# Optimization experiments

Measured on AMD Instinct MI355X. Metric: run time of the kernel, lower is better.

## Reference

```python
import jax, jax.numpy as jnp
import numpy as np
from jax import lax

B, T, H, F, K, NB, MAXLEN = 32, 1024, 384, 384, 3, 256, 2048


def _ln(x, g, b, eps=1e-5):
    m = jnp.mean(x, axis=-1, keepdims=True)
    v = jnp.var(x, axis=-1, keepdims=True)
    return (x - m) * lax.rsqrt(v + eps) * g + b


def _conv(x, w, b):
    # x: (B, T, Cin), w: (K, Cin, Cout); SAME padding == torch padding=(K-1)//2 for K=3, stride 1
    y = lax.conv_general_dilated(x, w, (1,), 'SAME', dimension_numbers=('NWC', 'WIO', 'NWC'))
    return y + b


def _predictor(x, mask, w1, b1, g1, be1, w2, b2, g2, be2, wo, bo):
    h = _ln(jax.nn.relu(_conv(x, w1, b1)), g1, be1)
    h = _ln(jax.nn.relu(_conv(h, w2, b2)), g2, be2)
    out = jnp.einsum('btf,f->bt', h, wo) + bo  # Linear(F -> 1).squeeze(-1)
    return jnp.where(mask, 0.0, out)


def _length_regulate(x, dur, max_len):
    # vectorized equivalent of torch per-sample expand+cat+pad
    csum = jnp.cumsum(dur, axis=1)                      # (B, T)
    total = csum[:, -1]                                 # (B,) = mel_len
    frames = jnp.arange(max_len)                        # (M,)
    # frame f belongs to phoneme i with csum[i-1] <= f < csum[i]
    idx = jax.vmap(lambda c: jnp.searchsorted(c, frames, side='right'))(csum)  # (B, M)
    idx = jnp.clip(idx, 0, x.shape[1] - 1)
    out = jnp.take_along_axis(x, idx[:, :, None], axis=1)                      # (B, M, H)
    valid = (frames[None, :] < total[:, None]).astype(x.dtype)                 # zero-pad tail
    return out * valid[:, :, None], total


def setup_inputs() -> dict:
    key = jax.random.key(0)
    ks = iter(jax.random.split(key, 64))
    nk = lambda: next(ks)
    d = {}
    d['x'] = jax.random.normal(nk(), (B, T, H), jnp.float32)
    d['src_mask'] = jnp.zeros((B, T), jnp.bool_)
    d['duration'] = jax.random.randint(nk(), (B, T), 0, 4)
    d['max_len'] = MAXLEN
    for p in ('dp', 'pp', 'ep'):
        d[p + '_w1'] = jax.random.normal(nk(), (K, H, F), jnp.float32) * 0.02
        d[p + '_b1'] = jnp.zeros((F,), jnp.float32)
        d[p + '_g1'] = jnp.ones((F,), jnp.float32)
        d[p + '_be1'] = jnp.zeros((F,), jnp.float32)
        d[p + '_w2'] = jax.random.normal(nk(), (K, F, F), jnp.float32) * 0.02
        d[p + '_b2'] = jnp.zeros((F,), jnp.float32)
        d[p + '_g2'] = jnp.ones((F,), jnp.float32)
        d[p + '_be2'] = jnp.zeros((F,), jnp.float32)
        d[p + '_wo'] = jax.random.normal(nk(), (F,), jnp.float32) * 0.02
        d[p + '_bo'] = jnp.zeros((1,), jnp.float32)
    d['pitch_bins'] = jnp.linspace(0.0, 1.0, NB - 1, dtype=jnp.float32)
    d['energy_bins'] = jnp.linspace(0.0, 1.0, NB - 1, dtype=jnp.float32)
    d['pitch_emb'] = jax.random.normal(nk(), (NB, H), jnp.float32) * 0.02
    d['energy_emb'] = jax.random.normal(nk(), (NB, H), jnp.float32) * 0.02
    d['pitch_target'] = jax.random.uniform(nk(), (B, T), jnp.float32)
    d['energy_target'] = jax.random.uniform(nk(), (B, T), jnp.float32)
    return d


def reference(x, src_mask, duration, max_len,
              dp_w1, dp_b1, dp_g1, dp_be1, dp_w2, dp_b2, dp_g2, dp_be2, dp_wo, dp_bo,
              pp_w1, pp_b1, pp_g1, pp_be1, pp_w2, pp_b2, pp_g2, pp_be2, pp_wo, pp_bo,
              ep_w1, ep_b1, ep_g1, ep_be1, ep_w2, ep_b2, ep_g2, ep_be2, ep_wo, ep_bo,
              pitch_bins, energy_bins, pitch_emb, energy_emb, pitch_target, energy_target):
    log_dur = _predictor(x, src_mask, dp_w1, dp_b1, dp_g1, dp_be1, dp_w2, dp_b2, dp_g2, dp_be2, dp_wo, dp_bo)
    # phoneme-level pitch (target path: bucketize target, torch.bucketize right=False == searchsorted left)
    pitch_pred = _predictor(x, src_mask, pp_w1, pp_b1, pp_g1, pp_be1, pp_w2, pp_b2, pp_g2, pp_be2, pp_wo, pp_bo)
    x = x + pitch_emb[jnp.searchsorted(pitch_bins, pitch_target, side='left')]
    # phoneme-level energy (predictor sees x AFTER pitch embedding add, as in torch)
    energy_pred = _predictor(x, src_mask, ep_w1, ep_b1, ep_g1, ep_be1, ep_w2, ep_b2, ep_g2, ep_be2, ep_wo, ep_bo)
    x = x + energy_emb[jnp.searchsorted(energy_bins, energy_target, side='left')]
    x_out, mel_len = _length_regulate(x, duration, max_len)
    return (x_out, pitch_pred, energy_pred, log_dur, mel_len)
```

## Files before the change

### kernel.cpp

```cpp
#include <hip/hip_runtime.h>

#define B_ 32
#define T_ 1024
#define C_ 384
#define MAXLEN_ 2048
#define NBINS_ 255
#define WPK1 442368
#define BTC  (32 * 1024 * 384)
#define ARS 392

typedef __attribute__((ext_vector_type(8))) short short8v;
typedef __attribute__((ext_vector_type(4))) float floatx4;

__device__ __forceinline__ unsigned short f2bf(float f) {
    unsigned u = __float_as_uint(f);
    u += 0x7fffu + ((u >> 16) & 1u);
    return (unsigned short)(u >> 16);
}

struct CvP {
    const float* xf;
    const unsigned short* xb;
    const unsigned short* wpk;
    const float* bias[3];
    const float* gamma[3];
    const float* beta[3];
    const float* wo[3];
    const float* bo[3];
    unsigned short* hout;
    float* pred[3];
    const float* pbins;
    const float* pemb;
    const float* ptgt;
    int final_flag;
};

__global__ __launch_bounds__(256, 2) void conv_mfma3(CvP P)
{
    __shared__ unsigned short As[66 * ARS];
    float* rsum = (float*)As;
    float* rsq  = rsum + 256;

    const int tid  = threadIdx.x;
    const int wave = tid >> 6;
    const int lane = tid & 63;
    const int lq   = lane >> 4;
    const int ln   = lane & 15;
    const int p    = blockIdx.x >> 9;
    const int bi   = blockIdx.x & 511;
    const int b    = bi >> 4;
    const int t0   = (bi & 15) << 6;
    const int nb   = wave * 96;

    const unsigned short* bbase =
        P.wpk + (size_t)p * WPK1 + wave * 3072 + (size_t)lane * 8;
    short8v bA[6], bB[6];
#pragma unroll
    for (int nt = 0; nt < 6; ++nt) {
        bA[nt] = *(const short8v*)(bbase + (nt << 9));
        bB[nt] = *(const short8v*)(bbase + 12288 + (nt << 9));
    }

    if (!P.final_flag) {
        const bool fuse_emb = (p == 2);
        for (int i = tid; i < 66 * 48; i += 256) {
            const int row = i / 48;
            const int c   = i - row * 48;
            const int t   = t0 - 1 + row;
            short8v v = (short8v){0,0,0,0,0,0,0,0};
            if ((unsigned)t < (unsigned)T_) {
                const float* sp = P.xf + ((size_t)(b << 10) + t) * C_ + c * 8;
                float f[8];
                *(float4*)&f[0] = *(const float4*)sp;
                *(float4*)&f[4] = *(const float4*)(sp + 4);
                if (fuse_emb) {
                    const float tg = P.ptgt[(b << 10) + t];
                    int lo = 0, hi = NBINS_;
                    while (lo < hi) {
                        const int mid = (lo + hi) >> 1;
                        if (P.pbins[mid] < tg) lo = mid + 1; else hi = mid;
                    }
                    const float* er = P.pemb + (size_t)lo * C_ + c * 8;
#pragma unroll
                    for (int j = 0; j < 8; ++j) f[j] += er[j];
                }
#pragma unroll
                for (int j = 0; j < 8; ++j) v[j] = (short)f2bf(f[j]);
            }
            *(short8v*)&As[row * ARS + c * 8] = v;
        }
    } else {
        const unsigned short* xb = P.xb + (size_t)p * BTC;
        for (int i = tid; i < 66 * 48; i += 256) {
            const int row = i / 48;
            const int c   = i - row * 48;
            const int t   = t0 - 1 + row;
            short8v v = (short8v){0,0,0,0,0,0,0,0};
            if ((unsigned)t < (unsigned)T_)
                v = *(const short8v*)(xb + ((size_t)(b << 10) + t) * C_ + c * 8);
            *(short8v*)&As[row * ARS + c * 8] = v;
        }
    }
    __syncthreads();

    floatx4 acc[24];
#pragma unroll
    for (int i = 0; i < 24; ++i) acc[i] = (floatx4){0.f, 0.f, 0.f, 0.f};

    const unsigned short* abase = &As[ln * ARS + lq * 8];
    const unsigned short* bpA = bbase + 2 * 12288;
    const unsigned short* bpB = bbase + 3 * 12288;

#pragma unroll
    for (int kc = 0; kc < 3; ++kc) {
#pragma unroll
        for (int h2 = 0; h2 < 6; ++h2) {
            const int hb = h2 * 64;
            const int r  = kc * 12 + h2 * 2;
            {
                short8v afrag[4];
#pragma unroll
                for (int mt = 0; mt < 4; ++mt)
                    afrag[mt] = *(const short8v*)(abase + (mt * 16 + kc) * ARS + hb);
#pragma unroll
                for (int mt = 0; mt < 4; ++mt)
#pragma unroll
                    for (int nt = 0; nt < 6; ++nt)
                        acc[mt * 6 + nt] = __builtin_amdgcn_mfma_f32_16x16x32_bf16(
                            afrag[mt], bA[nt], acc[mt * 6 + nt], 0, 0, 0);
                if (r + 2 < 36) {
#pragma unroll
                    for (int nt = 0; nt < 6; ++nt)
                        bA[nt] = *(const short8v*)(bpA + (nt << 9));
                    bpA += 24576;
                }
            }
            {
                short8v afrag[4];
#pragma unroll
                for (int mt = 0; mt < 4; ++mt)
                    afrag[mt] = *(const short8v*)(abase + (mt * 16 + kc) * ARS + hb + 32);
#pragma unroll
                for (int mt = 0; mt < 4; ++mt)
#pragma unroll
                    for (int nt = 0; nt < 6; ++nt)
                        acc[mt * 6 + nt] = __builtin_amdgcn_mfma_f32_16x16x32_bf16(
                            afrag[mt], bB[nt], acc[mt * 6 + nt], 0, 0, 0);
                if (r + 3 < 36) {
#pragma unroll
                    for (int nt = 0; nt < 6; ++nt)
                        bB[nt] = *(const short8v*)(bpB + (nt << 9));
                    bpB += 24576;
                }
            }
        }
    }
    __syncthreads();

    float bcol[6], gcol[6], becol[6], wcol[6];
#pragma unroll
    for (int nt = 0; nt < 6; ++nt) {
        const int col = nb + nt * 16 + ln;
        bcol[nt]  = P.bias[p][col];
        gcol[nt]  = P.gamma[p][col];
        becol[nt] = P.beta[p][col];
        wcol[nt]  = P.final_flag ? P.wo[p][col] : 0.f;
    }

#pragma unroll
    for (int mt = 0; mt < 4; ++mt) {
#pragma unroll
        for (int rg = 0; rg < 4; ++rg) {
            float s = 0.f, q = 0.f;
#pragma unroll
            for (int nt = 0; nt < 6; ++nt) {
                float v = acc[mt * 6 + nt][rg] + bcol[nt];
                v = v > 0.f ? v : 0.f;
                acc[mt * 6 + nt][rg] = v;
                s += v; q += v * v;
            }
#pragma unroll
            for (int off = 1; off < 16; off <<= 1) {
                s += __shfl_xor(s, off, 64);
                q += __shfl_xor(q, off, 64);
            }
            if (ln == mt * 4 + rg) {
                rsum[wave * 64 + mt * 16 + lq * 4 + rg] = s;
                rsq [wave * 64 + mt * 16 + lq * 4 + rg] = q;
            }
        }
    }
    __syncthreads();

    float mean_[16], rstd_[16];
#pragma unroll
    for (int mt = 0; mt < 4; ++mt) {
#pragma unroll
        for (int rg = 0; rg < 4; ++rg) {
            const int row = mt * 16 + lq * 4 + rg;
            const float s = rsum[row] + rsum[64 + row] + rsum[128 + row] + rsum[192 + row];
            const float q = rsq[row] + rsq[64 + row] + rsq[128 + row] + rsq[192 + row];
            const float m = s * (1.f / 384.f);
            const float var = q * (1.f / 384.f) - m * m;
            mean_[mt * 4 + rg] = m;
            rstd_[mt * 4 + rg] = rsqrtf(var + 1e-5f);
        }
    }

    if (!P.final_flag) {
        unsigned short* hout = P.hout + (size_t)p * BTC;
#pragma unroll
        for (int mt = 0; mt < 4; ++mt)
#pragma unroll
            for (int rg = 0; rg < 4; ++rg) {
                const float m = mean_[mt * 4 + rg], rs = rstd_[mt * 4 + rg];
                const int grow = (bi << 6) + mt * 16 + lq * 4 + rg;
#pragma unroll
                for (int nt = 0; nt < 6; ++nt) {
                    const float v = (acc[mt * 6 + nt][rg] - m) * rs * gcol[nt] + becol[nt];
                    hout[(size_t)grow * C_ + nb + nt * 16 + ln] = f2bf(v);
                }
            }
    } else {
        __syncthreads();
#pragma unroll
        for (int mt = 0; mt < 4; ++mt) {
#pragma unroll
            for (int rg = 0; rg < 4; ++rg) {
                const float m = mean_[mt * 4 + rg], rs = rstd_[mt * 4 + rg];
                float pr = 0.f;
#pragma unroll
                for (int nt = 0; nt < 6; ++nt)
                    pr += ((acc[mt * 6 + nt][rg] - m) * rs * gcol[nt] + becol[nt]) * wcol[nt];
#pragma unroll
                for (int off = 1; off < 16; off <<= 1)
                    pr += __shfl_xor(pr, off, 64);
                if (ln == mt * 4 + rg)
                    rsum[wave * 64 + mt * 16 + lq * 4 + rg] = pr;
            }
        }
        __syncthreads();
        if (tid < 64)
            P.pred[p][(bi << 6) + tid] =
                rsum[tid] + rsum[64 + tid] + rsum[128 + tid] + rsum[192 + tid] + P.bo[p][0];
    }
}

__global__ __launch_bounds__(256) void pack_w_kernel(
    const float* __restrict__ s0, const float* __restrict__ s1,
    const float* __restrict__ s2, const float* __restrict__ s3,
    const float* __restrict__ s4, const float* __restrict__ s5,
    unsigned short* __restrict__ dst)
{
    const int wsel = blockIdx.y;
    const float* src = wsel == 0 ? s0 : wsel == 1 ? s1 : wsel == 2 ? s2
                     : wsel == 3 ? s3 : wsel == 4 ? s4 : s5;
    const int o = blockIdx.x * 256 + threadIdx.x;
    const int r    = o / 12288;
    const int rem  = o - r * 12288;
    const int wv   = rem / 3072;
    const int rem2 = rem - wv * 3072;
    const int nt   = rem2 >> 9;
    const int li   = rem2 & 511;
    const int lane = li >> 3;
    const int j    = li & 7;
    const int n = wv * 96 + nt * 16 + (lane & 15);
    const int k = ((lane >> 4) << 3) + j;
    dst[(size_t)wsel * WPK1 + o] = f2bf(src[(size_t)(r * 32 + k) * C_ + n]);
}

__global__ __launch_bounds__(256) void cumsum_kernel(
    const int* __restrict__ dur, int* __restrict__ csum,
    float* __restrict__ mel_len)
{
    __shared__ int part[256];
    const int b = blockIdx.x;
    const int tid = threadIdx.x;
    int l[4];
    int s = 0;
#pragma unroll
    for (int i = 0; i < 4; ++i) { l[i] = dur[b * T_ + tid * 4 + i]; s += l[i]; }
    part[tid] = s;
    __syncthreads();
    for (int off = 1; off < 256; off <<= 1) {
        int u = 0;
        if (tid >= off) u = part[tid - off];
        __syncthreads();
        part[tid] += u;
        __syncthreads();
    }
    const int incl = part[tid];
    int run = incl - s;
#pragma unroll
    for (int i = 0; i < 4; ++i) {
        run += l[i];
        csum[b * T_ + tid * 4 + i] = run;
    }
    if (tid == 255) mel_len[b] = (float)incl;
}

__global__ __launch_bounds__(256) void length_reg_kernel(
    const float* __restrict__ x, const int* __restrict__ csum,
    const float* __restrict__ pbins, const float* __restrict__ pemb,
    const float* __restrict__ ptgt,
    const float* __restrict__ ebins, const float* __restrict__ eemb,
    const float* __restrict__ etgt,
    float* __restrict__ out)
{
    const int g    = blockIdx.x * 256 + threadIdx.x;
    const int c4   = g % 96;
    const int rest = g / 96;
    const int frame = rest & (MAXLEN_ - 1);
    const int b     = rest >> 11;
    const int* cr = csum + (b << 10);
    const int total = cr[T_ - 1];
    float4 v = make_float4(0.f, 0.f, 0.f, 0.f);
    if (frame < total) {
        int lo = 0, hi = T_;
        while (lo < hi) {
            const int mid = (lo + hi) >> 1;
            if (cr[mid] <= frame) lo = mid + 1; else hi = mid;
        }
        const int t = lo > T_ - 1 ? T_ - 1 : lo;
        const int row = (b << 10) + t;
        v = *(const float4*)(x + (size_t)row * C_ + c4 * 4);
        const float ptg = ptgt[row];
        int plo = 0, phi = NBINS_;
        while (plo < phi) {
            const int mid = (plo + phi) >> 1;
            if (pbins[mid] < ptg) plo = mid + 1; else phi = mid;
        }
        const float etg = etgt[row];
        int elo = 0, ehi = NBINS_;
        while (elo < ehi) {
            const int mid = (elo + ehi) >> 1;
            if (ebins[mid] < etg) elo = mid + 1; else ehi = mid;
        }
        const float4 pe = *(const float4*)(pemb + (size_t)plo * C_ + c4 * 4);
        const float4 ee = *(const float4*)(eemb + (size_t)elo * C_ + c4 * 4);
        v.x += pe.x + ee.x; v.y += pe.y + ee.y;
        v.z += pe.z + ee.z; v.w += pe.w + ee.w;
    }
    *(float4*)(out + (size_t)g * 4) = v;
}

extern "C" void kernel_launch(void* const* d_in, const int* in_sizes, int n_in,
                              void* d_out, int out_size, void* d_ws, size_t ws_size,
                              hipStream_t stream)
{
    const float* x        = (const float*)d_in[0];
    const int*   duration = (const int*)d_in[2];
    const float* P[3][10];
    for (int p = 0; p < 3; ++p)
        for (int q = 0; q < 10; ++q)
            P[p][q] = (const float*)d_in[4 + p * 10 + q];
    const float* pitch_bins    = (const float*)d_in[34];
    const float* energy_bins   = (const float*)d_in[35];
    const float* pitch_emb     = (const float*)d_in[36];
    const float* energy_emb    = (const float*)d_in[37];
    const float* pitch_target  = (const float*)d_in[38];
    const float* energy_target = (const float*)d_in[39];

    float* out_x      = (float*)d_out;
    float* out_pitch  = out_x + (size_t)B_ * MAXLEN_ * C_;
    float* out_energy = out_pitch + B_ * T_;
    float* out_logdur = out_energy + B_ * T_;
    float* out_mellen = out_logdur + B_ * T_;

    unsigned short* h1b = (unsigned short*)out_x;

    unsigned short* wpk = (unsigned short*)d_ws;
    int* csum = (int*)(wpk + (size_t)6 * WPK1);

    const dim3 blk(256);

    pack_w_kernel<<<dim3(1728, 6), blk, 0, stream>>>(
        P[0][0], P[0][4], P[1][0], P[1][4], P[2][0], P[2][4], wpk);

    CvP P1;
    P1.xf = x; P1.xb = nullptr; P1.wpk = wpk;
    for (int p = 0; p < 3; ++p) {
        P1.bias[p]  = P[p][1];
        P1.gamma[p] = P[p][2];
        P1.beta[p]  = P[p][3];
        P1.wo[p]    = nullptr;
        P1.bo[p]    = nullptr;
        P1.pred[p]  = nullptr;
    }
    P1.hout = h1b;
    P1.pbins = pitch_bins; P1.pemb = pitch_emb; P1.ptgt = pitch_target;
    P1.final_flag = 0;

    CvP P2;
    P2.xf = nullptr; P2.xb = h1b; P2.wpk = wpk + (size_t)3 * WPK1;
    for (int p = 0; p < 3; ++p) {
        P2.bias[p]  = P[p][5];
        P2.gamma[p] = P[p][6];
        P2.beta[p]  = P[p][7];
        P2.wo[p]    = P[p][8];
        P2.bo[p]    = P[p][9];
    }
    P2.pred[0] = out_logdur; P2.pred[1] = out_pitch; P2.pred[2] = out_energy;
    P2.hout = nullptr;
    P2.pbins = nullptr; P2.pemb = nullptr; P2.ptgt = nullptr;
    P2.final_flag = 1;

    conv_mfma3<<<1536, blk, 0, stream>>>(P1);
    conv_mfma3<<<1536, blk, 0, stream>>>(P2);

    cumsum_kernel<<<B_, blk, 0, stream>>>(duration, csum, out_mellen);
    length_reg_kernel<<<24576, blk, 0, stream>>>(
        x, csum, pitch_bins, pitch_emb, pitch_target,
        energy_bins, energy_emb, energy_target, out_x);
}
```

Baseline: 502.0 us.

## Single-buffer B fragments per column tile to raise occupancy to three blocks per CU

Replaces the double-buffered B-fragment registers (bA/bB) with one set that is refilled per column tile right after its MFMAs, roughly halving B register use. The launch bound rises to 3 blocks per CU to exploit the lower register pressure. The LDS row stride moves from 392 to 396 shorts to change the bank-conflict pattern. In exchange, weight loads are issued closer to their use, which gives less latency hiding within a wave and relies on the extra occupancy to cover it.

```diff
diff --git a/kernel.cpp b/kernel.cpp
--- a/kernel.cpp
+++ b/kernel.cpp
@@ -7,7 +7,7 @@
 #define NBINS_ 255
 #define WPK1 442368
 #define BTC  (32 * 1024 * 384)
-#define ARS 392
+#define ARS 396
 
 typedef __attribute__((ext_vector_type(8))) short short8v;
 typedef __attribute__((ext_vector_type(4))) float floatx4;
@@ -35,7 +35,7 @@
     int final_flag;
 };
 
-__global__ __launch_bounds__(256, 2) void conv_mfma3(CvP P)
+__global__ __launch_bounds__(256, 3) void conv_mfma3(CvP P)
 {
     __shared__ unsigned short As[66 * ARS];
     float* rsum = (float*)As;
@@ -54,12 +54,10 @@
 
     const unsigned short* bbase =
         P.wpk + (size_t)p * WPK1 + wave * 3072 + (size_t)lane * 8;
-    short8v bA[6], bB[6];
-#pragma unroll
-    for (int nt = 0; nt < 6; ++nt) {
-        bA[nt] = *(const short8v*)(bbase + (nt << 9));
-        bB[nt] = *(const short8v*)(bbase + 12288 + (nt << 9));
-    }
+    short8v bcur[6];
+#pragma unroll
+    for (int nt = 0; nt < 6; ++nt)
+        bcur[nt] = *(const short8v*)(bbase + (nt << 9));
 
     if (!P.final_flag) {
         const bool fuse_emb = (p == 2);
@@ -108,51 +106,28 @@
     for (int i = 0; i < 24; ++i) acc[i] = (floatx4){0.f, 0.f, 0.f, 0.f};
 
     const unsigned short* abase = &As[ln * ARS + lq * 8];
-    const unsigned short* bpA = bbase + 2 * 12288;
-    const unsigned short* bpB = bbase + 3 * 12288;
+    const unsigned short* bp = bbase + 12288;
 
 #pragma unroll
     for (int kc = 0; kc < 3; ++kc) {
 #pragma unroll
-        for (int h2 = 0; h2 < 6; ++h2) {
-            const int hb = h2 * 64;
-            const int r  = kc * 12 + h2 * 2;
-            {
-                short8v afrag[4];
+        for (int hh = 0; hh < 12; ++hh) {
+            const int r  = kc * 12 + hh;
+            const int hb = hh * 32;
+            short8v afrag[4];
+#pragma unroll
+            for (int mt = 0; mt < 4; ++mt)
+                afrag[mt] = *(const short8v*)(abase + (mt * 16 + kc) * ARS + hb);
+#pragma unroll
+            for (int nt = 0; nt < 6; ++nt) {
 #pragma unroll
                 for (int mt = 0; mt < 4; ++mt)
-                    afrag[mt] = *(const short8v*)(abase + (mt * 16 + kc) * ARS + hb);
-#pragma unroll
-                for (int mt = 0; mt < 4; ++mt)
-#pragma unroll
-                    for (int nt = 0; nt < 6; ++nt)
-                        acc[mt * 6 + nt] = __builtin_amdgcn_mfma_f32_16x16x32_bf16(
-                            afrag[mt], bA[nt], acc[mt * 6 + nt], 0, 0, 0);
-                if (r + 2 < 36) {
-#pragma unroll
-                    for (int nt = 0; nt < 6; ++nt)
-                        bA[nt] = *(const short8v*)(bpA + (nt << 9));
-                    bpA += 24576;
-                }
-            }
-            {
-                short8v afrag[4];
-#pragma unroll
-                for (int mt = 0; mt < 4; ++mt)
-                    afrag[mt] = *(const short8v*)(abase + (mt * 16 + kc) * ARS + hb + 32);
-#pragma unroll
-                for (int mt = 0; mt < 4; ++mt)
-#pragma unroll
-                    for (int nt = 0; nt < 6; ++nt)
-                        acc[mt * 6 + nt] = __builtin_amdgcn_mfma_f32_16x16x32_bf16(
-                            afrag[mt], bB[nt], acc[mt * 6 + nt], 0, 0, 0);
-                if (r + 3 < 36) {
-#pragma unroll
-                    for (int nt = 0; nt < 6; ++nt)
-                        bB[nt] = *(const short8v*)(bpB + (nt << 9));
-                    bpB += 24576;
-                }
-            }
+                    acc[mt * 6 + nt] = __builtin_amdgcn_mfma_f32_16x16x32_bf16(
+                        afrag[mt], bcur[nt], acc[mt * 6 + nt], 0, 0, 0);
+                if (r + 1 < 36)
+                    bcur[nt] = *(const short8v*)(bp + (nt << 9));
+            }
+            bp += 12288;
         }
     }
     __syncthreads();
```

New measurement: 586.5 us. 1.17x slower.

## Split conv tile across 8 waves and precompute length-regulator gather indices

Applied to the files above, without the earlier changes.

The conv kernel now runs 512 threads per block, with each of 8 waves owning 48 output columns instead of 96. This halves the accumulators per thread so more waves can be resident to hide latency, and the LDS row stride is padded differently. The cumsum kernel now does the frame-to-phoneme and bucketize binary searches once per frame and packs the results into an index buffer. The length-regulate kernel then only gathers, instead of repeating the searches for each of the 96 column threads. The cost is LayerNorm reductions over 8 partials and an extra index buffer in the workspace.

```diff
diff --git a/kernel.cpp b/kernel.cpp
--- a/kernel.cpp
+++ b/kernel.cpp
@@ -7,7 +7,7 @@
 #define NBINS_ 255
 #define WPK1 442368
 #define BTC  (32 * 1024 * 384)
-#define ARS 392
+#define ARS 396
 
 typedef __attribute__((ext_vector_type(8))) short short8v;
 typedef __attribute__((ext_vector_type(4))) float floatx4;
@@ -35,11 +35,11 @@
     int final_flag;
 };
 
-__global__ __launch_bounds__(256, 2) void conv_mfma3(CvP P)
+__global__ __launch_bounds__(512, 4) void conv_mfma3(CvP P)
 {
     __shared__ unsigned short As[66 * ARS];
     float* rsum = (float*)As;
-    float* rsq  = rsum + 256;
+    float* rsq  = rsum + 512;
 
     const int tid  = threadIdx.x;
     const int wave = tid >> 6;
@@ -50,20 +50,20 @@
     const int bi   = blockIdx.x & 511;
     const int b    = bi >> 4;
     const int t0   = (bi & 15) << 6;
-    const int nb   = wave * 96;
-
-    const unsigned short* bbase =
-        P.wpk + (size_t)p * WPK1 + wave * 3072 + (size_t)lane * 8;
-    short8v bA[6], bB[6];
-#pragma unroll
-    for (int nt = 0; nt < 6; ++nt) {
+    const int nb   = wave * 48;
+
+    const unsigned short* bbase = P.wpk + (size_t)p * WPK1
+        + (wave >> 1) * 3072 + (wave & 1) * 1536 + (size_t)lane * 8;
+    short8v bA[3], bB[3];
+#pragma unroll
+    for (int nt = 0; nt < 3; ++nt) {
         bA[nt] = *(const short8v*)(bbase + (nt << 9));
         bB[nt] = *(const short8v*)(bbase + 12288 + (nt << 9));
     }
 
     if (!P.final_flag) {
         const bool fuse_emb = (p == 2);
-        for (int i = tid; i < 66 * 48; i += 256) {
+        for (int i = tid; i < 66 * 48; i += 512) {
             const int row = i / 48;
             const int c   = i - row * 48;
             const int t   = t0 - 1 + row;
@@ -91,7 +91,7 @@
         }
     } else {
         const unsigned short* xb = P.xb + (size_t)p * BTC;
-        for (int i = tid; i < 66 * 48; i += 256) {
+        for (int i = tid; i < 66 * 48; i += 512) {
             const int row = i / 48;
             const int c   = i - row * 48;
             const int t   = t0 - 1 + row;
@@ -103,9 +103,9 @@
     }
     __syncthreads();
 
-    floatx4 acc[24];
-#pragma unroll
-    for (int i = 0; i < 24; ++i) acc[i] = (floatx4){0.f, 0.f, 0.f, 0.f};
+    floatx4 acc[12];
+#pragma unroll
+    for (int i = 0; i < 12; ++i) acc[i] = (floatx4){0.f, 0.f, 0.f, 0.f};
 
     const unsigned short* abase = &As[ln * ARS + lq * 8];
     const unsigned short* bpA = bbase + 2 * 12288;
@@ -125,12 +125,12 @@
 #pragma unroll
                 for (int mt = 0; mt < 4; ++mt)
 #pragma unroll
-                    for (int nt = 0; nt < 6; ++nt)
-                        acc[mt * 6 + nt] = __builtin_amdgcn_mfma_f32_16x16x32_bf16(
-                            afrag[mt], bA[nt], acc[mt * 6 + nt], 0, 0, 0);
+                    for (int nt = 0; nt < 3; ++nt)
+                        acc[mt * 3 + nt] = __builtin_amdgcn_mfma_f32_16x16x32_bf16(
+                            afrag[mt], bA[nt], acc[mt * 3 + nt], 0, 0, 0);
                 if (r + 2 < 36) {
 #pragma unroll
-                    for (int nt = 0; nt < 6; ++nt)
+                    for (int nt = 0; nt < 3; ++nt)
                         bA[nt] = *(const short8v*)(bpA + (nt << 9));
                     bpA += 24576;
                 }
@@ -143,12 +143,12 @@
 #pragma unroll
                 for (int mt = 0; mt < 4; ++mt)
 #pragma unroll
-                    for (int nt = 0; nt < 6; ++nt)
-                        acc[mt * 6 + nt] = __builtin_amdgcn_mfma_f32_16x16x32_bf16(
-                            afrag[mt], bB[nt], acc[mt * 6 + nt], 0, 0, 0);
+                    for (int nt = 0; nt < 3; ++nt)
+                        acc[mt * 3 + nt] = __builtin_amdgcn_mfma_f32_16x16x32_bf16(
+                            afrag[mt], bB[nt], acc[mt * 3 + nt], 0, 0, 0);
                 if (r + 3 < 36) {
 #pragma unroll
-                    for (int nt = 0; nt < 6; ++nt)
+                    for (int nt = 0; nt < 3; ++nt)
                         bB[nt] = *(const short8v*)(bpB + (nt << 9));
                     bpB += 24576;
                 }
@@ -157,9 +157,9 @@
     }
     __syncthreads();
 
-    float bcol[6], gcol[6], becol[6], wcol[6];
-#pragma unroll
-    for (int nt = 0; nt < 6; ++nt) {
+    float bcol[3], gcol[3], becol[3], wcol[3];
+#pragma unroll
+    for (int nt = 0; nt < 3; ++nt) {
         const int col = nb + nt * 16 + ln;
         bcol[nt]  = P.bias[p][col];
         gcol[nt]  = P.gamma[p][col];
@@ -173,10 +173,10 @@
         for (int rg = 0; rg < 4; ++rg) {
             float s = 0.f, q = 0.f;
 #pragma unroll
-            for (int nt = 0; nt < 6; ++nt) {
-                float v = acc[mt * 6 + nt][rg] + bcol[nt];
+            for (int nt = 0; nt < 3; ++nt) {
+                float v = acc[mt * 3 + nt][rg] + bcol[nt];
                 v = v > 0.f ? v : 0.f;
-                acc[mt * 6 + nt][rg] = v;
+                acc[mt * 3 + nt][rg] = v;
                 s += v; q += v * v;
             }
 #pragma unroll
@@ -198,8 +198,9 @@
 #pragma unroll
         for (int rg = 0; rg < 4; ++rg) {
             const int row = mt * 16 + lq * 4 + rg;
-            const float s = rsum[row] + rsum[64 + row] + rsum[128 + row] + rsum[192 + row];
-            const float q = rsq[row] + rsq[64 + row] + rsq[128 + row] + rsq[192 + row];
+            float s = 0.f, q = 0.f;
+#pragma unroll
+            for (int w = 0; w < 8; ++w) { s += rsum[w * 64 + row]; q += rsq[w * 64 + row]; }
             const float m = s * (1.f / 384.f);
             const float var = q * (1.f / 384.f) - m * m;
             mean_[mt * 4 + rg] = m;
@@ -216,8 +217,8 @@
                 const float m = mean_[mt * 4 + rg], rs = rstd_[mt * 4 + rg];
                 const int grow = (bi << 6) + mt * 16 + lq * 4 + rg;
 #pragma unroll
-                for (int nt = 0; nt < 6; ++nt) {
-                    const float v = (acc[mt * 6 + nt][rg] - m) * rs * gcol[nt] + becol[nt];
+                for (int nt = 0; nt < 3; ++nt) {
+                    const float v = (acc[mt * 3 + nt][rg] - m) * rs * gcol[nt] + becol[nt];
                     hout[(size_t)grow * C_ + nb + nt * 16 + ln] = f2bf(v);
                 }
             }
@@ -230,8 +231,8 @@
                 const float m = mean_[mt * 4 + rg], rs = rstd_[mt * 4 + rg];
                 float pr = 0.f;
 #pragma unroll
-                for (int nt = 0; nt < 6; ++nt)
-                    pr += ((acc[mt * 6 + nt][rg] - m) * rs * gcol[nt] + becol[nt]) * wcol[nt];
+                for (int nt = 0; nt < 3; ++nt)
+                    pr += ((acc[mt * 3 + nt][rg] - m) * rs * gcol[nt] + becol[nt]) * wcol[nt];
 #pragma unroll
                 for (int off = 1; off < 16; off <<= 1)
                     pr += __shfl_xor(pr, off, 64);
@@ -240,9 +241,12 @@
             }
         }
         __syncthreads();
-        if (tid < 64)
-            P.pred[p][(bi << 6) + tid] =
-                rsum[tid] + rsum[64 + tid] + rsum[128 + tid] + rsum[192 + tid] + P.bo[p][0];
+        if (tid < 64) {
+            float s = P.bo[p][0];
+#pragma unroll
+            for (int w = 0; w < 8; ++w) s += rsum[w * 64 + tid];
+            P.pred[p][(bi << 6) + tid] = s;
+        }
     }
 }
 
@@ -269,17 +273,22 @@
     dst[(size_t)wsel * WPK1 + o] = f2bf(src[(size_t)(r * 32 + k) * C_ + n]);
 }
 
-__global__ __launch_bounds__(256) void cumsum_kernel(
-    const int* __restrict__ dur, int* __restrict__ csum,
-    float* __restrict__ mel_len)
+__global__ __launch_bounds__(256) void cumsum_idx_kernel(
+    const int* __restrict__ dur,
+    const float* __restrict__ pbins, const float* __restrict__ ptgt,
+    const float* __restrict__ ebins, const float* __restrict__ etgt,
+    int* __restrict__ xidx, float* __restrict__ mel_len)
 {
+    __shared__ int cs[T_];
     __shared__ int part[256];
+    __shared__ float pb[NBINS_], eb[NBINS_];
     const int b = blockIdx.x;
     const int tid = threadIdx.x;
+    if (tid < NBINS_) { pb[tid] = pbins[tid]; eb[tid] = ebins[tid]; }
     int l[4];
     int s = 0;
 #pragma unroll
-    for (int i = 0; i < 4; ++i) { l[i] = dur[b * T_ + tid * 4 + i]; s += l[i]; }
+    for (int i = 0; i < 4; ++i) { l[i] = dur[(b << 10) + tid * 4 + i]; s += l[i]; }
     part[tid] = s;
     __syncthreads();
     for (int off = 1; off < 256; off <<= 1) {
@@ -294,17 +303,42 @@
 #pragma unroll
     for (int i = 0; i < 4; ++i) {
         run += l[i];
-        csum[b * T_ + tid * 4 + i] = run;
+        cs[tid * 4 + i] = run;
     }
     if (tid == 255) mel_len[b] = (float)incl;
+    __syncthreads();
+    const int total = cs[T_ - 1];
+    for (int f = tid; f < MAXLEN_; f += 256) {
+        int pk = -1;
+        if (f < total) {
+            int lo = 0, hi = T_;
+            while (lo < hi) {
+                const int mid = (lo + hi) >> 1;
+                if (cs[mid] <= f) lo = mid + 1; else hi = mid;
+            }
+            const int t = lo > T_ - 1 ? T_ - 1 : lo;
+            const int row = (b << 10) + t;
+            const float ptg = ptgt[row];
+            int plo = 0, phi = NBINS_;
+            while (plo < phi) {
+                const int mid = (plo + phi) >> 1;
+                if (pb[mid] < ptg) plo = mid + 1; else phi = mid;
+            }
+            const float etg = etgt[row];
+            int elo = 0, ehi = NBINS_;
+            while (elo < ehi) {
+                const int mid = (elo + ehi) >> 1;
+                if (eb[mid] < etg) elo = mid + 1; else ehi = mid;
+            }
+            pk = t | (plo << 10) | (elo << 19);
+        }
+        xidx[(b << 11) + f] = pk;
+    }
 }
 
 __global__ __launch_bounds__(256) void length_reg_kernel(
-    const float* __restrict__ x, const int* __restrict__ csum,
-    const float* __restrict__ pbins, const float* __restrict__ pemb,
-    const float* __restrict__ ptgt,
-    const float* __restrict__ ebins, const float* __restrict__ eemb,
-    const float* __restrict__ etgt,
+    const float* __restrict__ x, const int* __restrict__ xidx,
+    const float* __restrict__ pemb, const float* __restrict__ eemb,
     float* __restrict__ out)
 {
     const int g    = blockIdx.x * 256 + threadIdx.x;
@@ -312,30 +346,13 @@
     const int rest = g / 96;
     const int frame = rest & (MAXLEN_ - 1);
     const int b     = rest >> 11;
-    const int* cr = csum + (b << 10);
-    const int total = cr[T_ - 1];
+    const int pk = xidx[(b << 11) + frame];
     float4 v = make_float4(0.f, 0.f, 0.f, 0.f);
-    if (frame < total) {
-        int lo = 0, hi = T_;
-        while (lo < hi) {
-            const int mid = (lo + hi) >> 1;
-            if (cr[mid] <= frame) lo = mid + 1; else hi = mid;
-        }
-        const int t = lo > T_ - 1 ? T_ - 1 : lo;
-        const int row = (b << 10) + t;
-        v = *(const float4*)(x + (size_t)row * C_ + c4 * 4);
-        const float ptg = ptgt[row];
-        int plo = 0, phi = NBINS_;
-        while (plo < phi) {
-            const int mid = (plo + phi) >> 1;
-            if (pbins[mid] < ptg) plo = mid + 1; else phi = mid;
-        }
-        const float etg = etgt[row];
-        int elo = 0, ehi = NBINS_;
-        while (elo < ehi) {
-            const int mid = (elo + ehi) >> 1;
-            if (ebins[mid] < etg) elo = mid + 1; else ehi = mid;
-        }
+    if (pk >= 0) {
+        const int t   = pk & 1023;
+        const int plo = (pk >> 10) & 511;
+        const int elo = (pk >> 19) & 511;
+        v = *(const float4*)(x + ((size_t)(b << 10) + t) * C_ + c4 * 4);
         const float4 pe = *(const float4*)(pemb + (size_t)plo * C_ + c4 * 4);
         const float4 ee = *(const float4*)(eemb + (size_t)elo * C_ + c4 * 4);
         v.x += pe.x + ee.x; v.y += pe.y + ee.y;
@@ -370,7 +387,7 @@
     unsigned short* h1b = (unsigned short*)out_x;
 
     unsigned short* wpk = (unsigned short*)d_ws;
-    int* csum = (int*)(wpk + (size_t)6 * WPK1);
+    int* xidx = (int*)(wpk + (size_t)6 * WPK1);
 
     const dim3 blk(256);
 
@@ -405,11 +422,12 @@
     P2.pbins = nullptr; P2.pemb = nullptr; P2.ptgt = nullptr;
     P2.final_flag = 1;
 
-    conv_mfma3<<<1536, blk, 0, stream>>>(P1);
-    conv_mfma3<<<1536, blk, 0, stream>>>(P2);
-
-    cumsum_kernel<<<B_, blk, 0, stream>>>(duration, csum, out_mellen);
+    conv_mfma3<<<1536, dim3(512), 0, stream>>>(P1);
+    conv_mfma3<<<1536, dim3(512), 0, stream>>>(P2);
+
+    cumsum_idx_kernel<<<B_, blk, 0, stream>>>(
+        duration, pitch_bins, pitch_target, energy_bins, energy_target,
+        xidx, out_mellen);
     length_reg_kernel<<<24576, blk, 0, stream>>>(
-        x, csum, pitch_bins, pitch_emb, pitch_target,
-        energy_bins, energy_emb, energy_target, out_x);
-}
+        x, xidx, pitch_emb, energy_emb, out_x);
+}
```

Result: slower. 759.5 us (+51.3%).

## Precompute per-frame gather indices once and coalesce weight packing via LDS

Applied to the files above, without the earlier changes.

The binary searches for frame-to-phoneme mapping and pitch/energy bucketization move out of the length-regulate kernel, which ran them for each of 96 channel chunks per frame. They now run once per frame in the cumsum kernel, which writes a packed index array. The gather kernel then only decodes that index and does the loads. Separately, weight packing stages a 32-row slab in shared memory so global reads are coalesced float4 and writes are 16-byte bf16 vectors, replacing strided scalar gathers.

```diff
diff --git a/kernel.cpp b/kernel.cpp
--- a/kernel.cpp
+++ b/kernel.cpp
@@ -246,40 +246,64 @@
     }
 }
 
+#define WSS 388
 __global__ __launch_bounds__(256) void pack_w_kernel(
     const float* __restrict__ s0, const float* __restrict__ s1,
     const float* __restrict__ s2, const float* __restrict__ s3,
     const float* __restrict__ s4, const float* __restrict__ s5,
     unsigned short* __restrict__ dst)
 {
-    const int wsel = blockIdx.y;
+    __shared__ float ws[32 * WSS];
+    const int blk  = blockIdx.x;
+    const int wsel = blk / 36;
+    const int r    = blk - wsel * 36;
     const float* src = wsel == 0 ? s0 : wsel == 1 ? s1 : wsel == 2 ? s2
                      : wsel == 3 ? s3 : wsel == 4 ? s4 : s5;
-    const int o = blockIdx.x * 256 + threadIdx.x;
-    const int r    = o / 12288;
-    const int rem  = o - r * 12288;
-    const int wv   = rem / 3072;
-    const int rem2 = rem - wv * 3072;
-    const int nt   = rem2 >> 9;
-    const int li   = rem2 & 511;
-    const int lane = li >> 3;
-    const int j    = li & 7;
-    const int n = wv * 96 + nt * 16 + (lane & 15);
-    const int k = ((lane >> 4) << 3) + j;
-    dst[(size_t)wsel * WPK1 + o] = f2bf(src[(size_t)(r * 32 + k) * C_ + n]);
-}
-
-__global__ __launch_bounds__(256) void cumsum_kernel(
-    const int* __restrict__ dur, int* __restrict__ csum,
-    float* __restrict__ mel_len)
+    const int tid = threadIdx.x;
+
+    const float* sb = src + (size_t)r * 32 * C_;
+    for (int i4 = tid; i4 < 3072; i4 += 256) {
+        const int k  = i4 / 96;
+        const int n4 = i4 - k * 96;
+        *(float4*)&ws[k * WSS + n4 * 4] = *(const float4*)(sb + (size_t)k * C_ + n4 * 4);
+    }
+    __syncthreads();
+
+    unsigned short* db = dst + (size_t)wsel * WPK1 + (size_t)r * 12288;
+    for (int c = tid; c < 1536; c += 256) {
+        const int lane = c & 63;
+        const int wnt  = c >> 6;
+        const int ln   = lane & 15;
+        const int lq   = lane >> 4;
+        const int n    = (wnt / 6) * 96 + (wnt % 6) * 16 + ln;
+        ushort4 o0, o1;
+        unsigned short e[8];
+#pragma unroll
+        for (int j = 0; j < 8; ++j)
+            e[j] = f2bf(ws[(lq * 8 + j) * WSS + n]);
+        o0 = make_ushort4(e[0], e[1], e[2], e[3]);
+        o1 = make_ushort4(e[4], e[5], e[6], e[7]);
+        *(ushort4*)(db + wnt * 512 + lane * 8)     = o0;
+        *(ushort4*)(db + wnt * 512 + lane * 8 + 4) = o1;
+    }
+}
+
+__global__ __launch_bounds__(256) void cumsum_idx_kernel(
+    const int* __restrict__ dur,
+    const float* __restrict__ pbins, const float* __restrict__ ptgt,
+    const float* __restrict__ ebins, const float* __restrict__ etgt,
+    int* __restrict__ xidx, float* __restrict__ mel_len)
 {
+    __shared__ int cs[T_];
     __shared__ int part[256];
+    __shared__ float pb[NBINS_], eb[NBINS_];
     const int b = blockIdx.x;
     const int tid = threadIdx.x;
+    if (tid < NBINS_) { pb[tid] = pbins[tid]; eb[tid] = ebins[tid]; }
     int l[4];
     int s = 0;
 #pragma unroll
-    for (int i = 0; i < 4; ++i) { l[i] = dur[b * T_ + tid * 4 + i]; s += l[i]; }
+    for (int i = 0; i < 4; ++i) { l[i] = dur[(b << 10) + tid * 4 + i]; s += l[i]; }
     part[tid] = s;
     __syncthreads();
     for (int off = 1; off < 256; off <<= 1) {
@@ -294,17 +318,42 @@
 #pragma unroll
     for (int i = 0; i < 4; ++i) {
         run += l[i];
-        csum[b * T_ + tid * 4 + i] = run;
+        cs[tid * 4 + i] = run;
     }
     if (tid == 255) mel_len[b] = (float)incl;
+    __syncthreads();
+    const int total = cs[T_ - 1];
+    for (int f = tid; f < MAXLEN_; f += 256) {
+        int pk = -1;
+        if (f < total) {
+            int lo = 0, hi = T_;
+            while (lo < hi) {
+                const int mid = (lo + hi) >> 1;
+                if (cs[mid] <= f) lo = mid + 1; else hi = mid;
+            }
+            const int t = lo > T_ - 1 ? T_ - 1 : lo;
+            const int row = (b << 10) + t;
+            const float ptg = ptgt[row];
+            int plo = 0, phi = NBINS_;
+            while (plo < phi) {
+                const int mid = (plo + phi) >> 1;
+                if (pb[mid] < ptg) plo = mid + 1; else phi = mid;
+            }
+            const float etg = etgt[row];
+            int elo = 0, ehi = NBINS_;
+            while (elo < ehi) {
+                const int mid = (elo + ehi) >> 1;
+                if (eb[mid] < etg) elo = mid + 1; else ehi = mid;
+            }
+            pk = t | (plo << 10) | (elo << 19);
+        }
+        xidx[(b << 11) + f] = pk;
+    }
 }
 
 __global__ __launch_bounds__(256) void length_reg_kernel(
-    const float* __restrict__ x, const int* __restrict__ csum,
-    const float* __restrict__ pbins, const float* __restrict__ pemb,
-    const float* __restrict__ ptgt,
-    const float* __restrict__ ebins, const float* __restrict__ eemb,
-    const float* __restrict__ etgt,
+    const float* __restrict__ x, const int* __restrict__ xidx,
+    const float* __restrict__ pemb, const float* __restrict__ eemb,
     float* __restrict__ out)
 {
     const int g    = blockIdx.x * 256 + threadIdx.x;
@@ -312,30 +361,13 @@
     const int rest = g / 96;
     const int frame = rest & (MAXLEN_ - 1);
     const int b     = rest >> 11;
-    const int* cr = csum + (b << 10);
-    const int total = cr[T_ - 1];
+    const int pk = xidx[(b << 11) + frame];
     float4 v = make_float4(0.f, 0.f, 0.f, 0.f);
-    if (frame < total) {
-        int lo = 0, hi = T_;
-        while (lo < hi) {
-            const int mid = (lo + hi) >> 1;
-            if (cr[mid] <= frame) lo = mid + 1; else hi = mid;
-        }
-        const int t = lo > T_ - 1 ? T_ - 1 : lo;
-        const int row = (b << 10) + t;
-        v = *(const float4*)(x + (size_t)row * C_ + c4 * 4);
-        const float ptg = ptgt[row];
-        int plo = 0, phi = NBINS_;
-        while (plo < phi) {
-            const int mid = (plo + phi) >> 1;
-            if (pbins[mid] < ptg) plo = mid + 1; else phi = mid;
-        }
-        const float etg = etgt[row];
-        int elo = 0, ehi = NBINS_;
-        while (elo < ehi) {
-            const int mid = (elo + ehi) >> 1;
-            if (ebins[mid] < etg) elo = mid + 1; else ehi = mid;
-        }
+    if (pk >= 0) {
+        const int t   = pk & 1023;
+        const int plo = (pk >> 10) & 511;
+        const int elo = (pk >> 19) & 511;
+        v = *(const float4*)(x + ((size_t)(b << 10) + t) * C_ + c4 * 4);
         const float4 pe = *(const float4*)(pemb + (size_t)plo * C_ + c4 * 4);
         const float4 ee = *(const float4*)(eemb + (size_t)elo * C_ + c4 * 4);
         v.x += pe.x + ee.x; v.y += pe.y + ee.y;
@@ -370,11 +402,11 @@
     unsigned short* h1b = (unsigned short*)out_x;
 
     unsigned short* wpk = (unsigned short*)d_ws;
-    int* csum = (int*)(wpk + (size_t)6 * WPK1);
+    int* xidx = (int*)(wpk + (size_t)6 * WPK1);
 
     const dim3 blk(256);
 
-    pack_w_kernel<<<dim3(1728, 6), blk, 0, stream>>>(
+    pack_w_kernel<<<216, blk, 0, stream>>>(
         P[0][0], P[0][4], P[1][0], P[1][4], P[2][0], P[2][4], wpk);
 
     CvP P1;
@@ -408,8 +440,9 @@
     conv_mfma3<<<1536, blk, 0, stream>>>(P1);
     conv_mfma3<<<1536, blk, 0, stream>>>(P2);
 
-    cumsum_kernel<<<B_, blk, 0, stream>>>(duration, csum, out_mellen);
+    cumsum_idx_kernel<<<B_, blk, 0, stream>>>(
+        duration, pitch_bins, pitch_target, energy_bins, energy_target,
+        xidx, out_mellen);
     length_reg_kernel<<<24576, blk, 0, stream>>>(
-        x, csum, pitch_bins, pitch_emb, pitch_target,
-        energy_bins, energy_emb, energy_target, out_x);
-}
+        x, xidx, pitch_emb, energy_emb, out_x);
+}
```

Result: faster. 465.3 us (-7.3%).
